# Optimization experiments

Hardware: AMD Instinct MI355X
Metric: run time of the kernel (lower is better)

The kernel has to match this reference:

```python
import jax, jax.numpy as jnp
import numpy as np

B, S, D, H = 2, 2048, 2048, 16
HD = D // H  # 128


def _rope_tables(seq_len, head_dim, base=10000.0):
    inv_freq = 1.0 / (base ** (np.arange(0, head_dim, 2, dtype=np.float32) / head_dim))
    t = np.arange(seq_len, dtype=np.float32)
    freqs = np.outer(t, inv_freq)  # [S, HD/2]
    return jnp.asarray(np.cos(freqs)), jnp.asarray(np.sin(freqs))


def setup_inputs() -> dict:
    key = jax.random.key(0)
    ks = jax.random.split(key, 5)
    std = 0.02
    inp = {
        "x": jax.random.normal(ks[0], (B, S, D), jnp.float32),
        "wq": jax.random.normal(ks[1], (D, D), jnp.float32) * std,
        "bq": jnp.zeros((D,), jnp.float32),
        "wk": jax.random.normal(ks[2], (D, D), jnp.float32) * std,
        "bk": jnp.zeros((D,), jnp.float32),
        "wv": jax.random.normal(ks[3], (D, D), jnp.float32) * std,
        "bv": jnp.zeros((D,), jnp.float32),
        "wo": jax.random.normal(ks[4], (D, D), jnp.float32) * std,
        "bo": jnp.zeros((D,), jnp.float32),
    }
    cos, sin = _rope_tables(S, HD)
    inp["freqs_cos"], inp["freqs_sin"] = cos, sin
    return inp


def _apply_rope(t, cos, sin):
    # t: [B,S,H,HD]; cos/sin: [S,HD/2] -> broadcast [1,S,1,HD/2]
    tp = t.reshape(*t.shape[:-1], HD // 2, 2)
    t1, t2 = tp[..., 0], tp[..., 1]
    c = cos[None, :, None, :]
    s = sin[None, :, None, :]
    out = jnp.stack([t1 * c - t2 * s, t1 * s + t2 * c], axis=-1)
    return out.reshape(t.shape)


def reference(x, wq, bq, wk, bk, wv, bv, wo, bo, freqs_cos, freqs_sin):
    b, s, d = x.shape
    q = (x @ wq.T + bq).reshape(b, s, H, HD)
    k = (x @ wk.T + bk).reshape(b, s, H, HD)
    v = (x @ wv.T + bv).reshape(b, s, H, HD)
    q = _apply_rope(q, freqs_cos, freqs_sin)
    k = _apply_rope(k, freqs_cos, freqs_sin)
    # causal SDPA: scores [B,H,S,S]
    scale = 1.0 / jnp.sqrt(jnp.asarray(HD, x.dtype))
    scores = jnp.einsum("bqhd,bkhd->bhqk", q, k) * scale
    causal = jnp.tril(jnp.ones((s, s), bool))
    scores = jnp.where(causal[None, None], scores, jnp.asarray(-1e30, scores.dtype))
    attn = jax.nn.softmax(scores.astype(jnp.float32), axis=-1).astype(x.dtype)
    out = jnp.einsum("bhqk,bkhd->bqhd", attn, v).reshape(b, s, d)
    return out @ wo.T + bo
```

## Files before the change

kernel.cpp:

```cpp
#include <hip/hip_runtime.h>


typedef __attribute__((ext_vector_type(8))) short short8;
typedef __attribute__((ext_vector_type(4))) float f32x4;
typedef __attribute__((ext_vector_type(16))) float f32x16;
typedef __attribute__((ext_vector_type(2))) unsigned short u16x2;
typedef __attribute__((ext_vector_type(4))) unsigned short u16x4;
typedef __attribute__((ext_vector_type(8))) unsigned short u16x8;

constexpr int Bc = 2, Sc = 2048, Dc = 2048, Hc = 16, HDc = 128;
constexpr int Mc = Bc * Sc;
constexpr int Nc = Dc, Kc = Dc;
constexpr int NT = Kc / 64;
constexpr float QSCL = 0.08838834764831845f * 1.4426950408889634f;

__device__ __forceinline__ unsigned short f2bf(float f) {
    union { float f; unsigned u; } x; x.f = f;
    unsigned r = x.u + 0x7FFFu + ((x.u >> 16) & 1u);
    return (unsigned short)(r >> 16);
}
__device__ __forceinline__ float bf2f(unsigned short u) {
    union { float f; unsigned u; } x; x.u = (unsigned)u << 16; return x.f;
}

__device__ __forceinline__ void g2lds16(const void* g, void* l) {
    __builtin_amdgcn_global_load_lds(
        (const __attribute__((address_space(1))) void*)g,
        (__attribute__((address_space(3))) void*)l, 16, 0, 0);
}

__device__ __forceinline__ void cvt_body(const float* __restrict__ in,
                                         unsigned short* __restrict__ out, int i) {
    f32x4 a = *((const f32x4*)in + (size_t)i * 2);
    f32x4 b = *((const f32x4*)in + (size_t)i * 2 + 1);
    u16x8 o;
    o[0] = f2bf(a[0]); o[1] = f2bf(a[1]); o[2] = f2bf(a[2]); o[3] = f2bf(a[3]);
    o[4] = f2bf(b[0]); o[5] = f2bf(b[1]); o[6] = f2bf(b[2]); o[7] = f2bf(b[3]);
    *((u16x8*)out + i) = o;
}

__global__ __launch_bounds__(256) void cvt_f32_bf16(
    const float* __restrict__ in, unsigned short* __restrict__ out, int n8) {
    int i = blockIdx.x * 256 + threadIdx.x;
    if (i >= n8) return;
    cvt_body(in, out, i);
}

__global__ __launch_bounds__(256) void cvt_batch(
    const float* __restrict__ x,  unsigned short* __restrict__ xo,
    const float* __restrict__ w0, unsigned short* __restrict__ o0,
    const float* __restrict__ w1, unsigned short* __restrict__ o1,
    const float* __restrict__ w2, unsigned short* __restrict__ o2,
    const float* __restrict__ w3, unsigned short* __restrict__ o3) {
    const int which = blockIdx.y;
    const float* in; unsigned short* out; int n8;
    if (which == 0)      { in = x;  out = xo; n8 = (Mc * Dc) / 8; }
    else if (which == 1) { in = w0; out = o0; n8 = (Dc * Dc) / 8; }
    else if (which == 2) { in = w1; out = o1; n8 = (Dc * Dc) / 8; }
    else if (which == 3) { in = w2; out = o2; n8 = (Dc * Dc) / 8; }
    else                 { in = w3; out = o3; n8 = (Dc * Dc) / 8; }
    int i = blockIdx.x * 256 + threadIdx.x;
    if (i >= n8) return;
    cvt_body(in, out, i);
}

#define G9_STAGE_A(tt, rr, ii) {                                               \
    int s_ = (ii) * 512 + tid, row_ = s_ >> 3, c_ = s_ & 7;                    \
    g2lds16(A + (size_t)(m0 + row_) * Kc + (tt) * 64 + ((c_ ^ (row_ & 7)) << 3), \
            &As[rr][(size_t)((ii) * 512 + (w << 6)) * 8]); }
#define G9_STAGE_B(tt, rr, ii) {                                               \
    int s_ = (ii) * 512 + tid, row_ = s_ >> 3, c_ = s_ & 7;                    \
    g2lds16(W + (size_t)(n0 + row_) * Kc + (tt) * 64 + ((c_ ^ (row_ & 7)) << 3), \
            &Bs[rr][(size_t)((ii) * 512 + (w << 6)) * 8]); }
#define G9_RD(rr, kk) { _Pragma("unroll")                                      \
    for (int i = 0; i < 4; ++i) {                                              \
        int ra = wm * 64 + i * 16 + lrow;                                      \
        af[i] = *(const short8*)&As[rr][ra * 64 + ((((kk)*4 + lhi) ^ (ra & 7)) << 3)]; \
        int rb = wn * 64 + i * 16 + lrow;                                      \
        bf[i] = *(const short8*)&Bs[rr][rb * 64 + ((((kk)*4 + lhi) ^ (rb & 7)) << 3)]; } }
#define G9_MFMA16 { _Pragma("unroll")                                          \
    for (int i = 0; i < 4; ++i)                                                \
        _Pragma("unroll")                                                      \
        for (int j = 0; j < 4; ++j)                                            \
            acc[i][j] = __builtin_amdgcn_mfma_f32_16x16x32_bf16(af[i], bf[j], acc[i][j], 0, 0, 0); }
#define G9_SYNC1 __builtin_amdgcn_s_barrier();                                 \
    asm volatile("s_waitcnt lgkmcnt(0)" ::: "memory");                         \
    __builtin_amdgcn_s_setprio(1);
#define G9_SYNC2 __builtin_amdgcn_s_setprio(0); __builtin_amdgcn_s_barrier();

template <int KIND>
__global__ __launch_bounds__(512, 2) void gemm9(
    const unsigned short* __restrict__ A, const unsigned short* __restrict__ W,
    const float* __restrict__ bq, const float* __restrict__ bk,
    const float* __restrict__ bv, const float* __restrict__ rc,
    const float* __restrict__ rs, void* __restrict__ oq,
    unsigned short* __restrict__ ok, unsigned short* __restrict__ ov) {
    __shared__ __align__(16) unsigned short As[3][256 * 64];
    __shared__ __align__(16) unsigned short Bs[3][128 * 64];
    const int tid = threadIdx.x;
    const int w = tid >> 6, l = tid & 63;
    const int wm = w >> 1, wn = w & 1;
    const int lrow = l & 15, lhi = l >> 4;
    const int m0 = blockIdx.y * 256, n0 = blockIdx.x * 128;

    f32x4 acc[4][4];
#pragma unroll
    for (int i = 0; i < 4; ++i)
#pragma unroll
        for (int j = 0; j < 4; ++j) acc[i][j] = (f32x4){0.f, 0.f, 0.f, 0.f};

#pragma unroll
    for (int ii = 0; ii < 4; ++ii) G9_STAGE_A(0, 0, ii);
    G9_STAGE_B(0, 0, 0); G9_STAGE_B(0, 0, 1);
#pragma unroll
    for (int ii = 0; ii < 4; ++ii) G9_STAGE_A(1, 1, ii);
    G9_STAGE_B(1, 1, 0); G9_STAGE_B(1, 1, 1);
    asm volatile("s_waitcnt vmcnt(6)" ::: "memory");
    __builtin_amdgcn_s_barrier();

    short8 af[4], bf[4];
    for (int t = 0; t < NT; ++t) {
        const int r = t % 3, rn = (t + 2) % 3;
        const bool st = (t + 2) < NT;
        G9_RD(r, 0);
        if (st) { G9_STAGE_A(t + 2, rn, 0); G9_STAGE_A(t + 2, rn, 1); G9_STAGE_A(t + 2, rn, 2); }
        G9_SYNC1; G9_MFMA16; G9_SYNC2;
        G9_RD(r, 1);
        if (st) {
            G9_STAGE_A(t + 2, rn, 3); G9_STAGE_B(t + 2, rn, 0); G9_STAGE_B(t + 2, rn, 1);
            asm volatile("s_waitcnt vmcnt(6)" ::: "memory");
        } else {
            asm volatile("s_waitcnt vmcnt(0)" ::: "memory");
        }
        G9_SYNC1; G9_MFMA16; G9_SYNC2;
    }

    const int mode = (KIND == 1) ? 3 : (n0 >> 11);
    const float* bias = (KIND == 1) ? bq : (mode == 0 ? bq : mode == 1 ? bk : bv);
#pragma unroll
    for (int i = 0; i < 4; ++i) {
#pragma unroll
        for (int j = 0; j < 4; ++j) {
            int gm0 = m0 + wm * 64 + i * 16 + lhi * 4;
            int gn  = n0 + wn * 64 + j * 16 + lrow;
            int gnl = gn & (Dc - 1);
            float bvv = bias[gnl];
            if (mode == 0 || mode == 1) {
                unsigned short* o = (unsigned short*)(mode == 0 ? oq : (void*)ok);
                int fi = (gn & (HDc - 1)) >> 1;
#pragma unroll
                for (int rr = 0; rr < 4; ++rr) {
                    int gm = gm0 + rr;
                    float v = acc[i][j][rr] + bvv;
                    float p = __shfl_xor(v, 1);
                    int pos = gm & (Sc - 1);
                    float cz = rc[pos * (HDc / 2) + fi];
                    float sz = rs[pos * (HDc / 2) + fi];
                    float ovv = (gn & 1) ? (p * sz + v * cz) : (v * cz - p * sz);
                    if (mode == 0) ovv *= QSCL;
                    o[(size_t)gm * Dc + gnl] = f2bf(ovv);
                }
            } else if (mode == 2) {
                int b = gm0 >> 11, sb = gm0 & (Sc - 1);
                u16x4 pk;
#pragma unroll
                for (int rr = 0; rr < 4; ++rr) pk[rr] = f2bf(acc[i][j][rr] + bvv);
                *(u16x4*)&ov[((size_t)b * Dc + gnl) * Sc + sb] = pk;
            } else {
                float* o = (float*)oq;
#pragma unroll
                for (int rr = 0; rr < 4; ++rr)
                    o[(size_t)(gm0 + rr) * Nc + gn] = acc[i][j][rr] + bvv;
            }
        }
    }
}

template <int MODE>
__global__ __launch_bounds__(256) void gemm_nt(
    const unsigned short* __restrict__ A, const unsigned short* __restrict__ W,
    const float* __restrict__ bias, const float* __restrict__ rc,
    const float* __restrict__ rs, void* __restrict__ outp) {
    __shared__ __align__(16) unsigned short As[128 * 64];
    __shared__ __align__(16) unsigned short Bs[128 * 64];
    const int tid = threadIdx.x;
    const int w = tid >> 6, l = tid & 63;
    const int wm = w >> 1, wn = w & 1;
    const int lrow = l & 15, lhi = l >> 4;
    const int m0 = blockIdx.y * 128, n0 = blockIdx.x * 128;

    f32x4 acc[4][4];
#pragma unroll
    for (int i = 0; i < 4; ++i)
#pragma unroll
        for (int j = 0; j < 4; ++j) acc[i][j] = (f32x4){0.f, 0.f, 0.f, 0.f};

    for (int k0 = 0; k0 < Kc; k0 += 64) {
        __syncthreads();
#pragma unroll
        for (int i = 0; i < 4; ++i) {
            int s = i * 256 + tid;
            int row = s >> 3, c = s & 7;
            int cg = (c ^ (row & 7)) * 8;
            g2lds16(A + (size_t)(m0 + row) * Kc + k0 + cg,
                    &As[(size_t)(i * 256 + (w << 6)) * 8]);
            g2lds16(W + (size_t)(n0 + row) * Kc + k0 + cg,
                    &Bs[(size_t)(i * 256 + (w << 6)) * 8]);
        }
        __syncthreads();
#pragma unroll
        for (int kk = 0; kk < 2; ++kk) {
            short8 af[4], bf[4];
#pragma unroll
            for (int i = 0; i < 4; ++i) {
                int ra = wm * 64 + i * 16 + lrow;
                af[i] = *(const short8*)&As[ra * 64 + (((kk * 4 + lhi) ^ (ra & 7)) << 3)];
                int rb = wn * 64 + i * 16 + lrow;
                bf[i] = *(const short8*)&Bs[rb * 64 + (((kk * 4 + lhi) ^ (rb & 7)) << 3)];
            }
#pragma unroll
            for (int i = 0; i < 4; ++i)
#pragma unroll
                for (int j = 0; j < 4; ++j)
                    acc[i][j] = __builtin_amdgcn_mfma_f32_16x16x32_bf16(
                        af[i], bf[j], acc[i][j], 0, 0, 0);
        }
    }

#pragma unroll
    for (int i = 0; i < 4; ++i) {
#pragma unroll
        for (int j = 0; j < 4; ++j) {
            int gm0 = m0 + wm * 64 + i * 16 + lhi * 4;
            int gn  = n0 + wn * 64 + j * 16 + lrow;
            float bv = bias[gn];
            if (MODE == 0 || MODE == 1) {
                unsigned short* o = (unsigned short*)outp;
                int fi = (gn & (HDc - 1)) >> 1;
#pragma unroll
                for (int r = 0; r < 4; ++r) {
                    int gm = gm0 + r;
                    float v = acc[i][j][r] + bv;
                    float p = __shfl_xor(v, 1);
                    int pos = gm & (Sc - 1);
                    float cz = rc[pos * (HDc / 2) + fi];
                    float sz = rs[pos * (HDc / 2) + fi];
                    float ov = (gn & 1) ? (p * sz + v * cz) : (v * cz - p * sz);
                    if (MODE == 0) ov *= QSCL;
                    o[(size_t)gm * Nc + gn] = f2bf(ov);
                }
            } else if (MODE == 2) {
                unsigned short* o = (unsigned short*)outp;
                int b = gm0 >> 11, sb = gm0 & (Sc - 1);
                u16x4 pk;
#pragma unroll
                for (int r = 0; r < 4; ++r) pk[r] = f2bf(acc[i][j][r] + bv);
                *(u16x4*)&o[((size_t)b * Dc + gn) * Sc + sb] = pk;
            } else {
                float* o = (float*)outp;
#pragma unroll
                for (int r = 0; r < 4; ++r)
                    o[(size_t)(gm0 + r) * Nc + gn] = acc[i][j][r] + bv;
            }
        }
    }
}

#define ATTN_STAGE(tt, kd, vd) {                                               \
    const unsigned short* Kt = Kbase + (size_t)(tt) * 64 * Dc;                 \
    const unsigned short* Vp = Vbase + (tt) * 64;                              \
    _Pragma("unroll")                                                          \
    for (int i_ = 0; i_ < 4; ++i_) {                                           \
        int p_ = i_ * 256 + tid;                                               \
        int rK = p_ >> 4, sK = p_ & 15;                                        \
        g2lds16(Kt + (size_t)rK * Dc + ((sK ^ (rK & 15)) << 3),                \
                (kd) + (i_ * 256 + (w << 6)) * 8);                             \
        int rV = p_ >> 3, sV = p_ & 7;                                         \
        g2lds16(Vp + (size_t)rV * Sc + ((sV ^ (rV & 7)) << 3),                 \
                (vd) + (i_ * 256 + (w << 6)) * 8);                             \
    } }

#define ATTN_PVSTEP(PC, HB, KS) {                                              \
    int X0, X1, Y0, Y1;                                                        \
    asm("v_cvt_pk_bf16_f32 %0, %1, %2" : "=v"(X0) : "v"(PC[HB+0]), "v"(PC[HB+1])); \
    asm("v_cvt_pk_bf16_f32 %0, %1, %2" : "=v"(X1) : "v"(PC[HB+2]), "v"(PC[HB+3])); \
    asm("v_cvt_pk_bf16_f32 %0, %1, %2" : "=v"(Y0) : "v"(PC[HB+4]), "v"(PC[HB+5])); \
    asm("v_cvt_pk_bf16_f32 %0, %1, %2" : "=v"(Y1) : "v"(PC[HB+6]), "v"(PC[HB+7])); \
    asm("v_permlane32_swap_b32 %0, %1" : "+v"(X0), "+v"(Y0));                  \
    asm("v_permlane32_swap_b32 %0, %1" : "+v"(X1), "+v"(Y1));                  \
    union { int i[4]; short8 s; } pf_;                                         \
    pf_.i[0] = X0; pf_.i[1] = X1; pf_.i[2] = Y0; pf_.i[3] = Y1;                \
    _Pragma("unroll")                                                          \
    for (int dc_ = 0; dc_ < 4; ++dc_) {                                        \
        int rr = 32 * dc_ + ql;                                                \
        short8 vf = *(const short8*)&Vbuf[rr * 64 + (((2*(KS)+Hh) ^ (rr & 7)) << 3)]; \
        accv[dc_] = __builtin_amdgcn_mfma_f32_32x32x16_bf16(vf, pf_.s, accv[dc_], 0, 0, 0); \
    } }

#define ATTN_TILE_BODY(Kbuf, Vbuf, kb0)                                        \
    {                                                                          \
        f32x16 a0 = (f32x16)(0.f), a1 = (f32x16)(0.f);                         \
        __builtin_amdgcn_s_setprio(1);                                         \
        _Pragma("unroll")                                                      \
        for (int dc = 0; dc < 8; ++dc) {                                       \
            int r0 = ql, r1 = 32 + ql, sl = dc * 2 + Hh;                       \
            short8 k0 = *(const short8*)&Kbuf[r0 * 128 + ((sl ^ (r0 & 15)) << 3)]; \
            short8 k1 = *(const short8*)&Kbuf[r1 * 128 + ((sl ^ (r1 & 15)) << 3)]; \
            a0 = __builtin_amdgcn_mfma_f32_32x32x16_bf16(k0, qf[dc], a0, 0, 0, 0); \
            a1 = __builtin_amdgcn_mfma_f32_32x32x16_bf16(k1, qf[dc], a1, 0, 0, 0); \
        }                                                                      \
        __builtin_amdgcn_s_setprio(0);                                         \
        if ((kb0) >= 2 * qt * 64) {                                            \
            _Pragma("unroll")                                                  \
            for (int r = 0; r < 16; ++r) {                                     \
                int kl = (r & 3) + 8 * (r >> 2) + 4 * Hh;                      \
                if ((kb0) + kl > qg)      a0[r] = -3.0e38f;                    \
                if ((kb0) + 32 + kl > qg) a1[r] = -3.0e38f;                    \
            }                                                                  \
        }                                                                      \
        float m8[8];                                                           \
        _Pragma("unroll")                                                      \
        for (int r = 0; r < 8; ++r)                                            \
            m8[r] = fmaxf(fmaxf(a0[r], a0[r + 8]), fmaxf(a1[r], a1[r + 8]));   \
        float m4a = fmaxf(m8[0], m8[1]), m4b = fmaxf(m8[2], m8[3]);            \
        float m4c = fmaxf(m8[4], m8[5]), m4d = fmaxf(m8[6], m8[7]);            \
        float pm = fmaxf(fmaxf(m4a, m4b), fmaxf(m4c, m4d));                    \
        pm = fmaxf(pm, __shfl_xor(pm, 32));                                    \
        if (!__all(pm - mrun <= 8.0f)) {                                       \
            float mnew = fmaxf(mrun, pm);                                      \
            float fs = exp2f(mrun - mnew);                                     \
            mrun = mnew;                                                       \
            lrun *= fs;                                                        \
            _Pragma("unroll")                                                  \
            for (int dc = 0; dc < 4; ++dc)                                     \
                _Pragma("unroll")                                              \
                for (int r = 0; r < 16; ++r) accv[dc][r] *= fs;                \
        }                                                                      \
        float p0[16], p1[16];                                                  \
        _Pragma("unroll")                                                      \
        for (int r = 0; r < 16; ++r) p0[r] = exp2f(a0[r] - mrun);              \
        _Pragma("unroll")                                                      \
        for (int r = 0; r < 16; ++r) p1[r] = exp2f(a1[r] - mrun);              \
        float s8[8];                                                           \
        _Pragma("unroll")                                                      \
        for (int r = 0; r < 8; ++r)                                            \
            s8[r] = (p0[r] + p0[r + 8]) + (p1[r] + p1[r + 8]);                 \
        float s4a = s8[0] + s8[1], s4b = s8[2] + s8[3];                        \
        float s4c = s8[4] + s8[5], s4d = s8[6] + s8[7];                        \
        float ps = (s4a + s4b) + (s4c + s4d);                                  \
        lrun += ps + __shfl_xor(ps, 32);                                       \
        __builtin_amdgcn_s_setprio(1);                                         \
        ATTN_PVSTEP(p0, 0, 0); ATTN_PVSTEP(p0, 8, 1);                          \
        ATTN_PVSTEP(p1, 0, 2); ATTN_PVSTEP(p1, 8, 3);                          \
        __builtin_amdgcn_s_setprio(0);                                         \
    }

__global__ __launch_bounds__(256, 2) void attn_part(
    const unsigned short* __restrict__ Q, const unsigned short* __restrict__ Kb,
    const unsigned short* __restrict__ Vt, unsigned short* __restrict__ O,
    unsigned short* __restrict__ pacc, float* __restrict__ pml) {
    __shared__ __align__(16) unsigned short Ks[2][64 * 128];
    __shared__ __align__(16) unsigned short Vs[2][128 * 64];
    const int tid = threadIdx.x;
    const int w = tid >> 6, l = tid & 63;
    const int ql = l & 31, Hh = l >> 5;
    const int bh = blockIdx.x;
    const int slot = blockIdx.y;
    int qt, part, np;
    if (slot < 16) { qt = 15 - (slot >> 1); part = slot & 1; np = 2; }
    else           { qt = 23 - slot;        part = 0;        np = 1; }
    const int nt   = 2 * qt + 2;
    const int tbeg = part ? (qt + 1) : 0;
    const int tend = (np == 2 && part == 0) ? (qt + 1) : nt;
    const int b = bh >> 4, h = bh & 15;

    const unsigned short* Kbase = Kb + ((size_t)b * Sc) * Dc + h * HDc;
    const unsigned short* Vbase = Vt + ((size_t)b * Dc + h * HDc) * Sc;

    const int qw0 = qt * 128 + w * 32;
    const int qg = qw0 + ql;

    short8 qf[8];
    {
        const unsigned short* qp = Q + ((size_t)(b * Sc + qg)) * Dc + h * HDc;
#pragma unroll
        for (int dc = 0; dc < 8; ++dc)
            qf[dc] = *(const short8*)(qp + dc * 16 + Hh * 8);
    }
    f32x16 accv[4];
#pragma unroll
    for (int i = 0; i < 4; ++i) accv[i] = (f32x16)(0.f);
    float mrun = -3.0e38f, lrun = 0.f;

    ATTN_STAGE(tbeg, Ks[0], Vs[0]);
    for (int t = tbeg; t < tend; ++t) {
        const int cur = (t - tbeg) & 1;
        if (t + 1 < tend) {
            ATTN_STAGE(t + 1, Ks[cur ^ 1], Vs[cur ^ 1]);
            asm volatile("s_waitcnt vmcnt(8)" ::: "memory");
        } else {
            asm volatile("s_waitcnt vmcnt(0)" ::: "memory");
        }
        __builtin_amdgcn_s_barrier();

        const unsigned short* Kbuf = Ks[cur];
        const unsigned short* Vbuf = Vs[cur];
        const int kb0 = t * 64;
        if (kb0 <= qw0 + 31) ATTN_TILE_BODY(Kbuf, Vbuf, kb0);
        __builtin_amdgcn_s_barrier();
    }

    if (np == 1) {
        float inv = 1.f / lrun;
        unsigned short* Op = O + ((size_t)(b * Sc + qg)) * Dc + h * HDc;
#pragma unroll
        for (int dc = 0; dc < 4; ++dc)
#pragma unroll
            for (int rg = 0; rg < 4; ++rg) {
                int d0 = 32 * dc + 8 * rg + 4 * Hh;
                u16x4 pk;
#pragma unroll
                for (int j = 0; j < 4; ++j) pk[j] = f2bf(accv[dc][rg * 4 + j] * inv);
                *(u16x4*)(Op + d0) = pk;
            }
    } else {
        const int jslot = ((bh << 3) + (qt - 8)) * 2 + part;
        unsigned short* pa = pacc + (size_t)jslot * (128 * 128) + (w * 32 + ql) * 128;
#pragma unroll
        for (int dc = 0; dc < 4; ++dc)
#pragma unroll
            for (int rg = 0; rg < 4; ++rg) {
                u16x4 pk;
#pragma unroll
                for (int j = 0; j < 4; ++j) pk[j] = f2bf(accv[dc][rg * 4 + j]);
                *(u16x4*)&pa[32 * dc + 8 * rg + 4 * Hh] = pk;
            }
        if (Hh == 0) {
            float* pm2 = pml + (size_t)jslot * 256 + (w * 32 + ql) * 2;
            pm2[0] = mrun; pm2[1] = lrun;
        }
    }
}

__global__ __launch_bounds__(256) void attn_combine(
    const unsigned short* __restrict__ pacc, const float* __restrict__ pml,
    unsigned short* __restrict__ O) {
    const int w = threadIdx.x >> 6, l = threadIdx.x & 63;
    const int idx = blockIdx.x * 4 + w;
    const int jp = idx >> 7, row = idx & 127;
    const int bh = jp >> 3, qt = (jp & 7) + 8;
    const int b = bh >> 4, h = bh & 15;
    const unsigned short* a0 = pacc + ((size_t)jp * 2) * (128 * 128) + row * 128;
    const unsigned short* a1 = a0 + 128 * 128;
    const float* ml0 = pml + ((size_t)jp * 2) * 256 + row * 2;
    const float* ml1 = ml0 + 256;
    float m0 = ml0[0], l0 = ml0[1], m1 = ml1[0], l1 = ml1[1];
    float M = fmaxf(m0, m1);
    float w0 = exp2f(m0 - M), w1 = exp2f(m1 - M);
    float inv = 1.f / (l0 * w0 + l1 * w1);
    int d = l * 2;
    u16x2 v0 = *(const u16x2*)&a0[d];
    u16x2 v1 = *(const u16x2*)&a1[d];
    u16x2 pk;
    pk[0] = f2bf((bf2f(v0[0]) * w0 + bf2f(v1[0]) * w1) * inv);
    pk[1] = f2bf((bf2f(v0[1]) * w0 + bf2f(v1[1]) * w1) * inv);
    int qrow = qt * 128 + row;
    *(u16x2*)(O + ((size_t)(b * Sc + qrow)) * Dc + h * HDc + d) = pk;
}

__global__ __launch_bounds__(256, 2) void attn_fwd5(
    const unsigned short* __restrict__ Q, const unsigned short* __restrict__ Kb,
    const unsigned short* __restrict__ Vt, unsigned short* __restrict__ O) {
    __shared__ __align__(16) unsigned short Ks[2][64 * 128];
    __shared__ __align__(16) unsigned short Vs[2][128 * 64];
    const int tid = threadIdx.x;
    const int w = tid >> 6, l = tid & 63;
    const int ql = l & 31, Hh = l >> 5;
    const int bh = blockIdx.x;
    const int y = blockIdx.y;
    const int qt = (y < 8) ? y : (23 - y);
    const int b = bh >> 4, h = bh & 15;

    const unsigned short* Kbase = Kb + ((size_t)b * Sc) * Dc + h * HDc;
    const unsigned short* Vbase = Vt + ((size_t)b * Dc + h * HDc) * Sc;

    const int qw0 = qt * 128 + w * 32;
    const int qg = qw0 + ql;

    short8 qf[8];
    {
        const unsigned short* qp = Q + ((size_t)(b * Sc + qg)) * Dc + h * HDc;
#pragma unroll
        for (int dc = 0; dc < 8; ++dc)
            qf[dc] = *(const short8*)(qp + dc * 16 + Hh * 8);
    }
    f32x16 accv[4];
#pragma unroll
    for (int i = 0; i < 4; ++i) accv[i] = (f32x16)(0.f);
    float mrun = -3.0e38f, lrun = 0.f;
    const int nt = 2 * qt + 2;

    ATTN_STAGE(0, Ks[0], Vs[0]);
    for (int t = 0; t < nt; ++t) {
        if (t + 1 < nt) {
            ATTN_STAGE(t + 1, Ks[(t + 1) & 1], Vs[(t + 1) & 1]);
            asm volatile("s_waitcnt vmcnt(8)" ::: "memory");
        } else {
            asm volatile("s_waitcnt vmcnt(0)" ::: "memory");
        }
        __builtin_amdgcn_s_barrier();

        const unsigned short* Kbuf = Ks[t & 1];
        const unsigned short* Vbuf = Vs[t & 1];
        const int kb0 = t * 64;
        if (kb0 <= qw0 + 31) ATTN_TILE_BODY(Kbuf, Vbuf, kb0);
        __builtin_amdgcn_s_barrier();
    }
    float inv = 1.f / lrun;
    unsigned short* Op = O + ((size_t)(b * Sc + qg)) * Dc + h * HDc;
#pragma unroll
    for (int dc = 0; dc < 4; ++dc)
#pragma unroll
        for (int rg = 0; rg < 4; ++rg) {
            int d0 = 32 * dc + 8 * rg + 4 * Hh;
            u16x4 pk;
#pragma unroll
            for (int j = 0; j < 4; ++j) pk[j] = f2bf(accv[dc][rg * 4 + j] * inv);
            *(u16x4*)(Op + d0) = pk;
        }
}

extern "C" void kernel_launch(void* const* d_in, const int* in_sizes, int n_in,
                              void* d_out, int out_size, void* d_ws, size_t ws_size,
                              hipStream_t stream) {
    const float* x  = (const float*)d_in[0];
    const float* wq = (const float*)d_in[1];
    const float* bq = (const float*)d_in[2];
    const float* wk = (const float*)d_in[3];
    const float* bk = (const float*)d_in[4];
    const float* wv = (const float*)d_in[5];
    const float* bv = (const float*)d_in[6];
    const float* wo = (const float*)d_in[7];
    const float* bo = (const float*)d_in[8];
    const float* rc = (const float*)d_in[9];
    const float* rs = (const float*)d_in[10];

    const size_t NE = (size_t)Mc * Dc;
    const size_t NW = (size_t)Dc * Dc;

    unsigned short* xb = (unsigned short*)d_ws;
    unsigned short* qb = xb + NE;
    unsigned short* kb = qb + NE;
    unsigned short* vt = kb + NE;
    unsigned short* wb = vt + NE;

    const int ne8 = (int)(NE / 8), nw8 = (int)(NW / 8);
    dim3 tb(256);
    const bool big_ws = ws_size >= (4 * NE + 4 * NW) * sizeof(unsigned short);

    if (big_ws) {
        unsigned short* wqb = wb;
        unsigned short* wkb = wb + NW;
        unsigned short* wvb = wb + 2 * NW;
        unsigned short* wob = wb + 3 * NW;
        unsigned short* pacc = wb;
        float* pml = (float*)(wb + 2 * NW);
        cvt_batch<<<dim3(ne8 / 256, 5), tb, 0, stream>>>(
            x, xb, wq, wqb, wk, wkb, wv, wvb, wo, wob);
        gemm9<0><<<dim3(Nc * 3 / 128, Mc / 256), dim3(512), 0, stream>>>(
            xb, wb, bq, bk, bv, rc, rs, qb, kb, vt);
        attn_part<<<dim3(Bc * Hc, 24), tb, 0, stream>>>(qb, kb, vt, xb, pacc, pml);
        attn_combine<<<dim3(32 * 8 * 128 / 4), tb, 0, stream>>>(pacc, pml, xb);
        gemm9<1><<<dim3(Nc / 128, Mc / 256), dim3(512), 0, stream>>>(
            xb, wob, bo, nullptr, nullptr, rc, rs, d_out, nullptr, nullptr);
    } else {
        dim3 gg(Nc / 128, Mc / 128);
        cvt_f32_bf16<<<dim3(ne8 / 256), tb, 0, stream>>>(x, xb, ne8);
        cvt_f32_bf16<<<dim3(nw8 / 256), tb, 0, stream>>>(wq, wb, nw8);
        gemm_nt<0><<<gg, tb, 0, stream>>>(xb, wb, bq, rc, rs, qb);
        cvt_f32_bf16<<<dim3(nw8 / 256), tb, 0, stream>>>(wk, wb, nw8);
        gemm_nt<1><<<gg, tb, 0, stream>>>(xb, wb, bk, rc, rs, kb);
        cvt_f32_bf16<<<dim3(nw8 / 256), tb, 0, stream>>>(wv, wb, nw8);
        gemm_nt<2><<<gg, tb, 0, stream>>>(xb, wb, bv, rc, rs, vt);
        attn_fwd5<<<dim3(Bc * Hc, 16), tb, 0, stream>>>(qb, kb, vt, xb);
        cvt_f32_bf16<<<dim3(nw8 / 256), tb, 0, stream>>>(wo, wb, nw8);
        gemm_nt<3><<<gg, tb, 0, stream>>>(xb, wb, bo, rc, rs, d_out);
    }
}
```

Baseline: 249.2 us.

## Restructure GEMM main loop to one barrier pair per K-tile with rotating buffers

The GEMM main loop is rewritten so each K-tile issues all its global-to-LDS stages up front, then one barrier, then reads both k-halves of A and B fragments before running 32 MFMAs in one prioritized block. The old loop split each tile into two halves, each with its own barrier pair. Modulo-3 buffer indexing is replaced by rotating pointers. This halves the barriers per tile and removes index arithmetic, at the cost of double the fragment registers and less interleaving of LDS reads with MFMAs.

```diff
diff --git a/kernel.cpp b/kernel.cpp
--- a/kernel.cpp
+++ b/kernel.cpp
@@ -64,32 +64,30 @@
     cvt_body(in, out, i);
 }
 
-#define G9_STAGE_A(tt, rr, ii) {                                               \
+#define G10_STAGE_A(tt, dst, ii) {                                             \
     int s_ = (ii) * 512 + tid, row_ = s_ >> 3, c_ = s_ & 7;                    \
     g2lds16(A + (size_t)(m0 + row_) * Kc + (tt) * 64 + ((c_ ^ (row_ & 7)) << 3), \
-            &As[rr][(size_t)((ii) * 512 + (w << 6)) * 8]); }
-#define G9_STAGE_B(tt, rr, ii) {                                               \
+            (unsigned short*)(dst) + ((ii) * 512 + (w << 6)) * 8); }
+#define G10_STAGE_B(tt, dst, ii) {                                             \
     int s_ = (ii) * 512 + tid, row_ = s_ >> 3, c_ = s_ & 7;                    \
     g2lds16(W + (size_t)(n0 + row_) * Kc + (tt) * 64 + ((c_ ^ (row_ & 7)) << 3), \
-            &Bs[rr][(size_t)((ii) * 512 + (w << 6)) * 8]); }
-#define G9_RD(rr, kk) { _Pragma("unroll")                                      \
+            (unsigned short*)(dst) + ((ii) * 512 + (w << 6)) * 8); }
+#define G10_RDA(src, kk, f) { _Pragma("unroll")                                \
     for (int i = 0; i < 4; ++i) {                                              \
         int ra = wm * 64 + i * 16 + lrow;                                      \
-        af[i] = *(const short8*)&As[rr][ra * 64 + ((((kk)*4 + lhi) ^ (ra & 7)) << 3)]; \
-        int rb = wn * 64 + i * 16 + lrow;                                      \
-        bf[i] = *(const short8*)&Bs[rr][rb * 64 + ((((kk)*4 + lhi) ^ (rb & 7)) << 3)]; } }
-#define G9_MFMA16 { _Pragma("unroll")                                          \
+        f[i] = *(const short8*)&(src)[ra * 64 + ((((kk)*4 + lhi) ^ (ra & 7)) << 3)]; } }
+#define G10_RDB(src, kk, f) { _Pragma("unroll")                                \
+    for (int j = 0; j < 4; ++j) {                                              \
+        int rb = wn * 64 + j * 16 + lrow;                                      \
+        f[j] = *(const short8*)&(src)[rb * 64 + ((((kk)*4 + lhi) ^ (rb & 7)) << 3)]; } }
+#define G10_MFMA16(fa, fb) { _Pragma("unroll")                                 \
     for (int i = 0; i < 4; ++i)                                                \
         _Pragma("unroll")                                                      \
         for (int j = 0; j < 4; ++j)                                            \
-            acc[i][j] = __builtin_amdgcn_mfma_f32_16x16x32_bf16(af[i], bf[j], acc[i][j], 0, 0, 0); }
-#define G9_SYNC1 __builtin_amdgcn_s_barrier();                                 \
-    asm volatile("s_waitcnt lgkmcnt(0)" ::: "memory");                         \
-    __builtin_amdgcn_s_setprio(1);
-#define G9_SYNC2 __builtin_amdgcn_s_setprio(0); __builtin_amdgcn_s_barrier();
+            acc[i][j] = __builtin_amdgcn_mfma_f32_16x16x32_bf16(fa[i], fb[j], acc[i][j], 0, 0, 0); }
 
 template <int KIND>
-__global__ __launch_bounds__(512, 2) void gemm9(
+__global__ __launch_bounds__(512, 2) void gemm10(
     const unsigned short* __restrict__ A, const unsigned short* __restrict__ W,
     const float* __restrict__ bq, const float* __restrict__ bk,
     const float* __restrict__ bv, const float* __restrict__ rc,
@@ -109,30 +107,38 @@
 #pragma unroll
         for (int j = 0; j < 4; ++j) acc[i][j] = (f32x4){0.f, 0.f, 0.f, 0.f};
 
-#pragma unroll
-    for (int ii = 0; ii < 4; ++ii) G9_STAGE_A(0, 0, ii);
-    G9_STAGE_B(0, 0, 0); G9_STAGE_B(0, 0, 1);
-#pragma unroll
-    for (int ii = 0; ii < 4; ++ii) G9_STAGE_A(1, 1, ii);
-    G9_STAGE_B(1, 1, 0); G9_STAGE_B(1, 1, 1);
+    const unsigned short *Ard = As[0], *An1 = As[1], *Ast = As[2];
+    const unsigned short *Brd = Bs[0], *Bn1 = Bs[1], *Bst = Bs[2];
+
+#pragma unroll
+    for (int ii = 0; ii < 4; ++ii) G10_STAGE_A(0, Ard, ii);
+    G10_STAGE_B(0, Brd, 0); G10_STAGE_B(0, Brd, 1);
+#pragma unroll
+    for (int ii = 0; ii < 4; ++ii) G10_STAGE_A(1, An1, ii);
+    G10_STAGE_B(1, Bn1, 0); G10_STAGE_B(1, Bn1, 1);
     asm volatile("s_waitcnt vmcnt(6)" ::: "memory");
     __builtin_amdgcn_s_barrier();
 
-    short8 af[4], bf[4];
+    short8 a0f[4], b0f[4], a1f[4], b1f[4];
     for (int t = 0; t < NT; ++t) {
-        const int r = t % 3, rn = (t + 2) % 3;
-        const bool st = (t + 2) < NT;
-        G9_RD(r, 0);
-        if (st) { G9_STAGE_A(t + 2, rn, 0); G9_STAGE_A(t + 2, rn, 1); G9_STAGE_A(t + 2, rn, 2); }
-        G9_SYNC1; G9_MFMA16; G9_SYNC2;
-        G9_RD(r, 1);
-        if (st) {
-            G9_STAGE_A(t + 2, rn, 3); G9_STAGE_B(t + 2, rn, 0); G9_STAGE_B(t + 2, rn, 1);
+        if (t + 2 < NT) {
+#pragma unroll
+            for (int ii = 0; ii < 4; ++ii) G10_STAGE_A(t + 2, Ast, ii);
+            G10_STAGE_B(t + 2, Bst, 0); G10_STAGE_B(t + 2, Bst, 1);
             asm volatile("s_waitcnt vmcnt(6)" ::: "memory");
         } else {
             asm volatile("s_waitcnt vmcnt(0)" ::: "memory");
         }
-        G9_SYNC1; G9_MFMA16; G9_SYNC2;
+        __builtin_amdgcn_s_barrier();
+        G10_RDA(Ard, 0, a0f); G10_RDB(Brd, 0, b0f);
+        G10_RDA(Ard, 1, a1f); G10_RDB(Brd, 1, b1f);
+        __builtin_amdgcn_s_setprio(1);
+        G10_MFMA16(a0f, b0f);
+        G10_MFMA16(a1f, b1f);
+        __builtin_amdgcn_s_setprio(0);
+        __builtin_amdgcn_s_barrier();
+        const unsigned short* ta = Ard; Ard = An1; An1 = Ast; Ast = ta;
+        const unsigned short* tb = Brd; Brd = Bn1; Bn1 = Bst; Bst = tb;
     }
 
     const int mode = (KIND == 1) ? 3 : (n0 >> 11);
@@ -567,11 +573,11 @@
         float* pml = (float*)(wb + 2 * NW);
         cvt_batch<<<dim3(ne8 / 256, 5), tb, 0, stream>>>(
             x, xb, wq, wqb, wk, wkb, wv, wvb, wo, wob);
-        gemm9<0><<<dim3(Nc * 3 / 128, Mc / 256), dim3(512), 0, stream>>>(
+        gemm10<0><<<dim3(Nc * 3 / 128, Mc / 256), dim3(512), 0, stream>>>(
             xb, wb, bq, bk, bv, rc, rs, qb, kb, vt);
         attn_part<<<dim3(Bc * Hc, 24), tb, 0, stream>>>(qb, kb, vt, xb, pacc, pml);
         attn_combine<<<dim3(32 * 8 * 128 / 4), tb, 0, stream>>>(pacc, pml, xb);
-        gemm9<1><<<dim3(Nc / 128, Mc / 256), dim3(512), 0, stream>>>(
+        gemm10<1><<<dim3(Nc / 128, Mc / 256), dim3(512), 0, stream>>>(
             xb, wob, bo, nullptr, nullptr, rc, rs, d_out, nullptr, nullptr);
     } else {
         dim3 gg(Nc / 128, Mc / 128);
```

After: 283.3 us. 13.7% more time.
